# Kernel optimization log

Measured on AMD Instinct MI355X. Metric: run time of the kernel, lower is better.

Reference implementation:

```python
import jax, jax.numpy as jnp
import numpy as np

B, S, C, H = 1, 512, 384, 12
SQK, SV, PQK, PV = 16, 16, 4, 8
SCALAR_SCALE = SQK ** -0.5
NEG = jnp.float32(-10000.0)


def _random_rotations(key, shape):
    # Gram-Schmidt on random normals -> proper rotation matrices (rows orthonormal)
    m = jax.random.normal(key, shape + (3, 3), jnp.float32)
    e0 = m[..., 0, :]
    e0 = e0 / jnp.linalg.norm(e0, axis=-1, keepdims=True)
    e1 = m[..., 1, :] - jnp.sum(e0 * m[..., 1, :], axis=-1, keepdims=True) * e0
    e1 = e1 / jnp.linalg.norm(e1, axis=-1, keepdims=True)
    e2 = jnp.cross(e0, e1)
    return jnp.stack([e0, e1, e2], axis=-2)  # [..., 3, 3]


def setup_inputs() -> dict:
    key = jax.random.key(0)
    ks = jax.random.split(key, 24)
    rn = lambda k, shp, s=1.0: jax.random.normal(k, shp, jnp.float32) * s
    w = 0.02  # weight init scale
    inp = {
        'single_repr': rn(ks[0], (B, S, C)),
        'rotations': _random_rotations(ks[1], (B, S)),
        'translations': rn(ks[2], (B, S, 3), 10.0),
        'Wq_s': rn(ks[3], (C, H * SQK), w), 'bq_s': rn(ks[4], (H * SQK,), w),
        'Wk_s': rn(ks[5], (C, H * SQK), w), 'bk_s': rn(ks[6], (H * SQK,), w),
        'Wv_s': rn(ks[7], (C, H * SV), w), 'bv_s': rn(ks[8], (H * SV,), w),
        'Wq_p': rn(ks[9], (C, H * PQK * 3), w), 'bq_p': rn(ks[10], (H * PQK * 3,), w),
        'Wk_p': rn(ks[11], (C, H * PQK * 3), w), 'bk_p': rn(ks[12], (H * PQK * 3,), w),
        'Wv_p': rn(ks[13], (C, H * PV * 3), w), 'bv_p': rn(ks[14], (H * PV * 3,), w),
        'point_weights': rn(ks[15], (H, PQK), 0.5),
        'Wo': rn(ks[16], (H * (SV + PV * 4), C), w), 'bo': rn(ks[17], (C,), w),
        'valid_mask': jax.random.randint(ks[18], (B, S), 0, 2).astype(bool),
    }
    return inp


def _ipa(single_repr, rotations, translations,
         Wq_s, bq_s, Wk_s, bk_s, Wv_s, bv_s,
         Wq_p, bq_p, Wk_p, bk_p, Wv_p, bv_p,
         point_weights, Wo, bo, valid_mask):
    b, s, _ = single_repr.shape
    qs = (single_repr @ Wq_s + bq_s).reshape(b, s, H, SQK)
    ks = (single_repr @ Wk_s + bk_s).reshape(b, s, H, SQK)
    vs = (single_repr @ Wv_s + bv_s).reshape(b, s, H, SV)
    qp = (single_repr @ Wq_p + bq_p).reshape(b, s, H, PQK, 3)
    kp = (single_repr @ Wk_p + bk_p).reshape(b, s, H, PQK, 3)
    vp = (single_repr @ Wv_p + bv_p).reshape(b, s, H, PV, 3)
    t = translations[:, :, None, None, :]
    # local -> global: R @ p + t
    qpg = jnp.einsum('bsij,bshpj->bshpi', rotations, qp) + t
    kpg = jnp.einsum('bsij,bshpj->bshpi', rotations, kp) + t
    vpg = jnp.einsum('bsij,bshpj->bshpi', rotations, vp) + t
    scalar_logits = jnp.einsum('bihd,bjhd->bhij', qs, ks) * SCALAR_SCALE
    # pairwise point distances: [b, i, j, h, p]
    delta = qpg[:, :, None] - kpg[:, None]  # [b, i, j, h, p, 3]
    dist2 = jnp.sum(delta * delta, axis=-1)
    sp_w = jax.nn.softplus(point_weights)  # [H, PQK]
    point_logits = -0.5 * jnp.einsum('bijhp,hp->bhij', dist2, sp_w)
    logits = scalar_logits + point_logits
    key_mask = valid_mask[:, None, None, :]
    logits = jnp.where(key_mask, logits, NEG)
    attn = jax.nn.softmax(logits, axis=-1)
    attn = attn * valid_mask[:, None, :, None].astype(attn.dtype)
    scalar_out = jnp.einsum('bhij,bjhd->bihd', attn, vs).reshape(b, s, H * SV)
    pog = jnp.einsum('bhij,bjhpd->bihpd', attn, vpg)  # [b, s, H, PV, 3]
    # global -> local: R^T (x - t)
    pol = jnp.einsum('bsji,bshpj->bshpi', rotations, pog - t)
    point_norm = jnp.sqrt(jnp.sum(pol * pol, axis=-1))  # [b, s, H, PV]
    combined = jnp.concatenate([
        scalar_out,
        pol.reshape(b, s, H * PV * 3),
        point_norm.reshape(b, s, H * PV),
    ], axis=-1)
    update = combined @ Wo + bo
    return update * valid_mask[..., None].astype(update.dtype)


def reference(single_repr, rotations, translations,
              Wq_s, bq_s, Wk_s, bk_s, Wv_s, bv_s,
              Wq_p, bq_p, Wk_p, bk_p, Wv_p, bv_p,
              point_weights, Wo, bo, valid_mask):
    return _ipa(single_repr, rotations, translations,
                Wq_s, bq_s, Wk_s, bk_s, Wv_s, bv_s,
                Wq_p, bq_p, Wk_p, bk_p, Wv_p, bv_p,
                point_weights, Wo, bo, valid_mask)
```

## Files before the change

kernel.cpp:

```cpp
#include <hip/hip_runtime.h>
#include <math.h>

#define S 512
#define C 384
#define H 12
#define SCALAR_SCALE 0.25f
#define NEG_LOGIT (-10000.0f)

#define XCOLS 1152
#define DQK 28
#define DV 40

__global__ __launch_bounds__(256)
void gemm_proj(const float* __restrict__ A,
               const float* __restrict__ Wq_s, const float* __restrict__ bq_s,
               const float* __restrict__ Wk_s, const float* __restrict__ bk_s,
               const float* __restrict__ Wv_s, const float* __restrict__ bv_s,
               const float* __restrict__ Wq_p, const float* __restrict__ bq_p,
               const float* __restrict__ Wk_p, const float* __restrict__ bk_p,
               const float* __restrict__ Wv_p, const float* __restrict__ bv_p,
               float* __restrict__ X)
{
    __shared__ float As[48][65];
    __shared__ float Bs[48][65];
    const int tid = threadIdx.x;
    const int m0 = blockIdx.y * 64;
    const int n0 = blockIdx.x * 64;
    const int ty = tid >> 4;
    const int tx = tid & 15;

    const int n = n0 + tx * 4;
    const float* bsrc; const float* bbias; int ldbs, ncol;
    if      (n < 192) { bsrc = Wq_s; bbias = bq_s; ldbs = 192; ncol = n; }
    else if (n < 384) { bsrc = Wk_s; bbias = bk_s; ldbs = 192; ncol = n - 192; }
    else if (n < 576) { bsrc = Wv_s; bbias = bv_s; ldbs = 192; ncol = n - 384; }
    else if (n < 720) { bsrc = Wq_p; bbias = bq_p; ldbs = 144; ncol = n - 576; }
    else if (n < 864) { bsrc = Wk_p; bbias = bk_p; ldbs = 144; ncol = n - 720; }
    else              { bsrc = Wv_p; bbias = bv_p; ldbs = 288; ncol = n - 864; }

    float acc[4][4] = {};

    for (int k0 = 0; k0 < C; k0 += 48) {
        {
            int r = tid >> 2;
            int cbase = (tid & 3) * 4;
            #pragma unroll
            for (int cc = 0; cc < 3; ++cc) {
                int c = cbase + cc * 16;
                const float4 v = *(const float4*)(A + (size_t)(m0 + r) * C + k0 + c);
                As[c + 0][r] = v.x; As[c + 1][r] = v.y;
                As[c + 2][r] = v.z; As[c + 3][r] = v.w;
            }
        }
        {
            int r = tid >> 4;
            int c = tx * 4;
            #pragma unroll
            for (int rr = 0; rr < 3; ++rr) {
                const float4 v = *(const float4*)(bsrc + (size_t)(k0 + r + rr * 16) * ldbs + ncol);
                Bs[r + rr * 16][c + 0] = v.x; Bs[r + rr * 16][c + 1] = v.y;
                Bs[r + rr * 16][c + 2] = v.z; Bs[r + rr * 16][c + 3] = v.w;
            }
        }
        __syncthreads();
        #pragma unroll
        for (int k = 0; k < 48; ++k) {
            float a[4], b[4];
            #pragma unroll
            for (int i = 0; i < 4; ++i) a[i] = As[k][ty * 4 + i];
            #pragma unroll
            for (int j = 0; j < 4; ++j) b[j] = Bs[k][tx * 4 + j];
            #pragma unroll
            for (int i = 0; i < 4; ++i)
                #pragma unroll
                for (int j = 0; j < 4; ++j)
                    acc[i][j] += a[i] * b[j];
        }
        __syncthreads();
    }

    const float4 bb = *(const float4*)(bbias + ncol);
    #pragma unroll
    for (int i = 0; i < 4; ++i) {
        int m = m0 + ty * 4 + i;
        float4 o = make_float4(acc[i][0] + bb.x, acc[i][1] + bb.y,
                               acc[i][2] + bb.z, acc[i][3] + bb.w);
        *(float4*)(X + (size_t)m * XCOLS + n) = o;
    }
}

__global__ __launch_bounds__(256)
void gemm_out(const float* __restrict__ A, int lda,
              const float* __restrict__ B, int ldb,
              const float* __restrict__ bias,
              float* __restrict__ Cc, int ldc, int K,
              const int* __restrict__ rowMask)
{
    __shared__ float As[32][33];
    __shared__ float Bs[32][33];
    const int tid = threadIdx.x;
    const int m0 = blockIdx.y * 32;
    const int n0 = blockIdx.x * 32;
    const int ty = tid >> 4;
    const int tx = tid & 15;

    float acc[2][2] = {};

    for (int k0 = 0; k0 < K; k0 += 32) {
        {
            int r = tid >> 3;
            int c = (tid & 7) * 4;
            const float4 v = *(const float4*)(A + (size_t)(m0 + r) * lda + k0 + c);
            As[c + 0][r] = v.x; As[c + 1][r] = v.y;
            As[c + 2][r] = v.z; As[c + 3][r] = v.w;
        }
        {
            int r = tid >> 3;
            int c = (tid & 7) * 4;
            const float4 v = *(const float4*)(B + (size_t)(k0 + r) * ldb + n0 + c);
            Bs[r][c + 0] = v.x; Bs[r][c + 1] = v.y;
            Bs[r][c + 2] = v.z; Bs[r][c + 3] = v.w;
        }
        __syncthreads();
        #pragma unroll
        for (int k = 0; k < 32; ++k) {
            float a0 = As[k][ty * 2], a1 = As[k][ty * 2 + 1];
            float b0 = Bs[k][tx * 2], b1 = Bs[k][tx * 2 + 1];
            acc[0][0] += a0 * b0; acc[0][1] += a0 * b1;
            acc[1][0] += a1 * b0; acc[1][1] += a1 * b1;
        }
        __syncthreads();
    }

    #pragma unroll
    for (int i = 0; i < 2; ++i) {
        int m = m0 + ty * 2 + i;
        float msk = rowMask[m] ? 1.0f : 0.0f;
        #pragma unroll
        for (int j = 0; j < 2; ++j) {
            int n = n0 + tx * 2 + j;
            Cc[(size_t)m * ldc + n] = (acc[i][j] + bias[n]) * msk;
        }
    }
}

__global__ __launch_bounds__(256)
void ipa_points(const float* __restrict__ X,
                const float* __restrict__ rot,
                const float* __restrict__ trans,
                const float* __restrict__ pw,
                float4* __restrict__ Q4, float4* __restrict__ K4,
                float4* __restrict__ V4, float* __restrict__ kb)
{
    int idx = blockIdx.x * 256 + threadIdx.x;
    int h = idx >> 9;
    int s = idx & 511;

    float R[9], t[3];
    #pragma unroll
    for (int i = 0; i < 9; ++i) R[i] = rot[s * 9 + i];
    #pragma unroll
    for (int i = 0; i < 3; ++i) t[i] = trans[s * 3 + i];

    float spw[4];
    #pragma unroll
    for (int p = 0; p < 4; ++p)
        spw[p] = log1pf(__expf(pw[h * 4 + p]));

    const float4* xr4 = (const float4*)(X + (size_t)s * XCOLS);

    float qv[DQK], kv[DQK], vv[DV];
    #pragma unroll
    for (int g = 0; g < 4; ++g) {
        float4 a = xr4[h * 4 + g];
        qv[g * 4 + 0] = a.x * SCALAR_SCALE; qv[g * 4 + 1] = a.y * SCALAR_SCALE;
        qv[g * 4 + 2] = a.z * SCALAR_SCALE; qv[g * 4 + 3] = a.w * SCALAR_SCALE;
        float4 b = xr4[48 + h * 4 + g];
        kv[g * 4 + 0] = b.x; kv[g * 4 + 1] = b.y; kv[g * 4 + 2] = b.z; kv[g * 4 + 3] = b.w;
        float4 c = xr4[96 + h * 4 + g];
        vv[g * 4 + 0] = c.x; vv[g * 4 + 1] = c.y; vv[g * 4 + 2] = c.z; vv[g * 4 + 3] = c.w;
    }
    float qp[12], kp[12], vp[24];
    #pragma unroll
    for (int g = 0; g < 3; ++g) {
        float4 a = xr4[144 + h * 3 + g];
        qp[g * 4 + 0] = a.x; qp[g * 4 + 1] = a.y; qp[g * 4 + 2] = a.z; qp[g * 4 + 3] = a.w;
        float4 b = xr4[180 + h * 3 + g];
        kp[g * 4 + 0] = b.x; kp[g * 4 + 1] = b.y; kp[g * 4 + 2] = b.z; kp[g * 4 + 3] = b.w;
    }
    #pragma unroll
    for (int g = 0; g < 6; ++g) {
        float4 a = xr4[216 + h * 6 + g];
        vp[g * 4 + 0] = a.x; vp[g * 4 + 1] = a.y; vp[g * 4 + 2] = a.z; vp[g * 4 + 3] = a.w;
    }

    float knorm = 0.0f;
    #pragma unroll
    for (int p = 0; p < 4; ++p) {
        #pragma unroll
        for (int i = 0; i < 3; ++i) {
            float qg = R[i * 3] * qp[p * 3] + R[i * 3 + 1] * qp[p * 3 + 1] + R[i * 3 + 2] * qp[p * 3 + 2] + t[i];
            float kg = R[i * 3] * kp[p * 3] + R[i * 3 + 1] * kp[p * 3 + 1] + R[i * 3 + 2] * kp[p * 3 + 2] + t[i];
            qv[16 + p * 3 + i] = spw[p] * qg;
            kv[16 + p * 3 + i] = kg;
            knorm += spw[p] * kg * kg;
        }
    }
    kb[(size_t)h * S + s] = -0.5f * knorm;

    #pragma unroll
    for (int p = 0; p < 8; ++p) {
        #pragma unroll
        for (int i = 0; i < 3; ++i)
            vv[16 + p * 3 + i] = R[i * 3] * vp[p * 3] + R[i * 3 + 1] * vp[p * 3 + 1] + R[i * 3 + 2] * vp[p * 3 + 2] + t[i];
    }

    #pragma unroll
    for (int g = 0; g < 7; ++g)
        Q4[((size_t)h * 7 + g) * S + s] = make_float4(qv[g * 4], qv[g * 4 + 1], qv[g * 4 + 2], qv[g * 4 + 3]);
    #pragma unroll
    for (int g = 0; g < 7; ++g)
        K4[((size_t)h * 7 + g) * S + s] = make_float4(kv[g * 4], kv[g * 4 + 1], kv[g * 4 + 2], kv[g * 4 + 3]);
    #pragma unroll
    for (int g = 0; g < 10; ++g)
        V4[((size_t)h * 10 + g) * S + s] = make_float4(vv[g * 4], vv[g * 4 + 1], vv[g * 4 + 2], vv[g * 4 + 3]);
}

__global__ __launch_bounds__(256)
void ipa_attn(const float4* __restrict__ Q4, const float4* __restrict__ K4,
              const float4* __restrict__ V4, const float* __restrict__ kb,
              const int* __restrict__ valid,
              const float* __restrict__ rot, const float* __restrict__ trans,
              float* __restrict__ combined)
{
    __shared__ float4 sh[4][10];
    const int h = blockIdx.x;
    const int wave = threadIdx.x >> 6;
    const int lane = threadIdx.x & 63;
    const int i = blockIdx.y * 4 + wave;

    float q[DQK];
    #pragma unroll
    for (int g = 0; g < 7; ++g) {
        float4 v = Q4[((size_t)h * 7 + g) * S + i];
        q[g * 4] = v.x; q[g * 4 + 1] = v.y; q[g * 4 + 2] = v.z; q[g * 4 + 3] = v.w;
    }

    const float* kbh = kb + (size_t)h * S;

    float logit[8];
    float mx = -3.0e38f;
    #pragma unroll
    for (int t = 0; t < 8; ++t) {
        int j = t * 64 + lane;
        float dot = kbh[j];
        #pragma unroll
        for (int g = 0; g < 7; ++g) {
            float4 k = K4[((size_t)h * 7 + g) * S + j];
            dot += q[g * 4] * k.x + q[g * 4 + 1] * k.y + q[g * 4 + 2] * k.z + q[g * 4 + 3] * k.w;
        }
        logit[t] = valid[j] ? dot : NEG_LOGIT;
        mx = fmaxf(mx, logit[t]);
    }
    #pragma unroll
    for (int off = 32; off >= 1; off >>= 1)
        mx = fmaxf(mx, __shfl_xor(mx, off, 64));

    float sum = 0.0f;
    #pragma unroll
    for (int t = 0; t < 8; ++t) {
        logit[t] = __expf(logit[t] - mx);
        sum += logit[t];
    }
    #pragma unroll
    for (int off = 32; off >= 1; off >>= 1)
        sum += __shfl_xor(sum, off, 64);
    const float inv = 1.0f / sum;

    float4 acc[10];
    #pragma unroll
    for (int g = 0; g < 10; ++g) acc[g] = make_float4(0.f, 0.f, 0.f, 0.f);
    #pragma unroll
    for (int t = 0; t < 8; ++t) {
        int j = t * 64 + lane;
        float p = logit[t];
        #pragma unroll
        for (int g = 0; g < 10; ++g) {
            float4 v = V4[((size_t)h * 10 + g) * S + j];
            acc[g].x += p * v.x; acc[g].y += p * v.y;
            acc[g].z += p * v.z; acc[g].w += p * v.w;
        }
    }
    #pragma unroll
    for (int g = 0; g < 10; ++g) {
        #pragma unroll
        for (int off = 32; off >= 1; off >>= 1) {
            acc[g].x += __shfl_xor(acc[g].x, off, 64);
            acc[g].y += __shfl_xor(acc[g].y, off, 64);
            acc[g].z += __shfl_xor(acc[g].z, off, 64);
            acc[g].w += __shfl_xor(acc[g].w, off, 64);
        }
    }

    if (lane == 0) {
        #pragma unroll
        for (int g = 0; g < 10; ++g) sh[wave][g] = acc[g];
    }
    const float* shf = (const float*)sh[wave];

    float* crow = combined + (size_t)i * 576;
    if (lane < 16)
        crow[h * 16 + lane] = shf[lane] * inv;

    if (lane < 8) {
        float R[9], t_[3];
        #pragma unroll
        for (int a = 0; a < 9; ++a) R[a] = rot[i * 9 + a];
        #pragma unroll
        for (int a = 0; a < 3; ++a) t_[a] = trans[i * 3 + a];
        int p = lane;
        float d0 = shf[16 + p * 3 + 0] * inv - t_[0];
        float d1 = shf[16 + p * 3 + 1] * inv - t_[1];
        float d2 = shf[16 + p * 3 + 2] * inv - t_[2];
        float pol0 = R[0] * d0 + R[3] * d1 + R[6] * d2;
        float pol1 = R[1] * d0 + R[4] * d1 + R[7] * d2;
        float pol2 = R[2] * d0 + R[5] * d1 + R[8] * d2;
        crow[192 + h * 24 + p * 3 + 0] = pol0;
        crow[192 + h * 24 + p * 3 + 1] = pol1;
        crow[192 + h * 24 + p * 3 + 2] = pol2;
        crow[480 + h * 8 + p] = sqrtf(pol0 * pol0 + pol1 * pol1 + pol2 * pol2);
    }
}

extern "C" void kernel_launch(void* const* d_in, const int* in_sizes, int n_in,
                              void* d_out, int out_size, void* d_ws, size_t ws_size,
                              hipStream_t stream)
{
    const float* single = (const float*)d_in[0];
    const float* rot    = (const float*)d_in[1];
    const float* trans  = (const float*)d_in[2];
    const float* Wq_s   = (const float*)d_in[3];
    const float* bq_s   = (const float*)d_in[4];
    const float* Wk_s   = (const float*)d_in[5];
    const float* bk_s   = (const float*)d_in[6];
    const float* Wv_s   = (const float*)d_in[7];
    const float* bv_s   = (const float*)d_in[8];
    const float* Wq_p   = (const float*)d_in[9];
    const float* bq_p   = (const float*)d_in[10];
    const float* Wk_p   = (const float*)d_in[11];
    const float* bk_p   = (const float*)d_in[12];
    const float* Wv_p   = (const float*)d_in[13];
    const float* bv_p   = (const float*)d_in[14];
    const float* pw     = (const float*)d_in[15];
    const float* Wo     = (const float*)d_in[16];
    const float* bo     = (const float*)d_in[17];
    const int*   valid  = (const int*)d_in[18];

    float* ws = (float*)d_ws;
    float* X        = ws;
    float* Q4f      = X + (size_t)S * XCOLS;
    float* K4f      = Q4f + (size_t)H * 7 * S * 4;
    float* V4f      = K4f + (size_t)H * 7 * S * 4;
    float* kbb      = V4f + (size_t)H * 10 * S * 4;
    float* combined = kbb + (size_t)H * S;

    dim3 blk(256);

    gemm_proj<<<dim3(XCOLS / 64, S / 64), blk, 0, stream>>>(
        single, Wq_s, bq_s, Wk_s, bk_s, Wv_s, bv_s,
        Wq_p, bq_p, Wk_p, bk_p, Wv_p, bv_p, X);

    ipa_points<<<dim3(S * H / 256), blk, 0, stream>>>(X, rot, trans, pw,
                                                      (float4*)Q4f, (float4*)K4f, (float4*)V4f, kbb);

    ipa_attn<<<dim3(H, S / 4), blk, 0, stream>>>((const float4*)Q4f, (const float4*)K4f,
                                                 (const float4*)V4f, kbb, valid, rot, trans, combined);

    gemm_out<<<dim3(C / 32, S / 32), blk, 0, stream>>>(combined, 576, Wo, C, bo, (float*)d_out, C, 576, valid);
}
```

Before: 189.3 us.

## Split-K projection GEMM with register prefetch; widen output GEMM K tile

Result: no change. 189.1 us (-0.1%).

```diff
diff --git a/kernel.cpp b/kernel.cpp
--- a/kernel.cpp
+++ b/kernel.cpp
@@ -19,13 +19,14 @@
                const float* __restrict__ Wq_p, const float* __restrict__ bq_p,
                const float* __restrict__ Wk_p, const float* __restrict__ bk_p,
                const float* __restrict__ Wv_p, const float* __restrict__ bv_p,
-               float* __restrict__ X)
+               float* __restrict__ X0)
 {
     __shared__ float As[48][65];
     __shared__ float Bs[48][65];
     const int tid = threadIdx.x;
     const int m0 = blockIdx.y * 64;
     const int n0 = blockIdx.x * 64;
+    const int z  = blockIdx.z;
     const int ty = tid >> 4;
     const int tx = tid & 15;
 
@@ -38,31 +39,51 @@
     else if (n < 864) { bsrc = Wk_p; bbias = bk_p; ldbs = 144; ncol = n - 720; }
     else              { bsrc = Wv_p; bbias = bv_p; ldbs = 288; ncol = n - 864; }
 
+    float* Xp = X0 + (size_t)z * S * XCOLS;
+
+    const int ar  = tid >> 2;
+    const int acb = (tid & 3) * 4;
+    const int br  = tid >> 4;
+
+    float4 rA[3], rB[3];
+    {
+        const int k0 = z * 192;
+        #pragma unroll
+        for (int cc = 0; cc < 3; ++cc)
+            rA[cc] = *(const float4*)(A + (size_t)(m0 + ar) * C + k0 + acb + cc * 16);
+        #pragma unroll
+        for (int rr = 0; rr < 3; ++rr)
+            rB[rr] = *(const float4*)(bsrc + (size_t)(k0 + br + rr * 16) * ldbs + ncol);
+    }
+
     float acc[4][4] = {};
 
-    for (int k0 = 0; k0 < C; k0 += 48) {
-        {
-            int r = tid >> 2;
-            int cbase = (tid & 3) * 4;
+    #pragma unroll
+    for (int it = 0; it < 4; ++it) {
+        #pragma unroll
+        for (int cc = 0; cc < 3; ++cc) {
+            int c = acb + cc * 16;
+            As[c + 0][ar] = rA[cc].x; As[c + 1][ar] = rA[cc].y;
+            As[c + 2][ar] = rA[cc].z; As[c + 3][ar] = rA[cc].w;
+        }
+        #pragma unroll
+        for (int rr = 0; rr < 3; ++rr) {
+            int c = tx * 4;
+            Bs[br + rr * 16][c + 0] = rB[rr].x; Bs[br + rr * 16][c + 1] = rB[rr].y;
+            Bs[br + rr * 16][c + 2] = rB[rr].z; Bs[br + rr * 16][c + 3] = rB[rr].w;
+        }
+        __syncthreads();
+
+        if (it < 3) {
+            const int kn = z * 192 + (it + 1) * 48;
             #pragma unroll
-            for (int cc = 0; cc < 3; ++cc) {
-                int c = cbase + cc * 16;
-                const float4 v = *(const float4*)(A + (size_t)(m0 + r) * C + k0 + c);
-                As[c + 0][r] = v.x; As[c + 1][r] = v.y;
-                As[c + 2][r] = v.z; As[c + 3][r] = v.w;
-            }
-        }
-        {
-            int r = tid >> 4;
-            int c = tx * 4;
+            for (int cc = 0; cc < 3; ++cc)
+                rA[cc] = *(const float4*)(A + (size_t)(m0 + ar) * C + kn + acb + cc * 16);
             #pragma unroll
-            for (int rr = 0; rr < 3; ++rr) {
-                const float4 v = *(const float4*)(bsrc + (size_t)(k0 + r + rr * 16) * ldbs + ncol);
-                Bs[r + rr * 16][c + 0] = v.x; Bs[r + rr * 16][c + 1] = v.y;
-                Bs[r + rr * 16][c + 2] = v.z; Bs[r + rr * 16][c + 3] = v.w;
-            }
-        }
-        __syncthreads();
+            for (int rr = 0; rr < 3; ++rr)
+                rB[rr] = *(const float4*)(bsrc + (size_t)(kn + br + rr * 16) * ldbs + ncol);
+        }
+
         #pragma unroll
         for (int k = 0; k < 48; ++k) {
             float a[4], b[4];
@@ -79,13 +100,22 @@
         __syncthreads();
     }
 
-    const float4 bb = *(const float4*)(bbias + ncol);
-    #pragma unroll
-    for (int i = 0; i < 4; ++i) {
-        int m = m0 + ty * 4 + i;
-        float4 o = make_float4(acc[i][0] + bb.x, acc[i][1] + bb.y,
-                               acc[i][2] + bb.z, acc[i][3] + bb.w);
-        *(float4*)(X + (size_t)m * XCOLS + n) = o;
+    if (z == 0) {
+        const float4 bb = *(const float4*)(bbias + ncol);
+        #pragma unroll
+        for (int i = 0; i < 4; ++i) {
+            int m = m0 + ty * 4 + i;
+            *(float4*)(Xp + (size_t)m * XCOLS + n) =
+                make_float4(acc[i][0] + bb.x, acc[i][1] + bb.y,
+                            acc[i][2] + bb.z, acc[i][3] + bb.w);
+        }
+    } else {
+        #pragma unroll
+        for (int i = 0; i < 4; ++i) {
+            int m = m0 + ty * 4 + i;
+            *(float4*)(Xp + (size_t)m * XCOLS + n) =
+                make_float4(acc[i][0], acc[i][1], acc[i][2], acc[i][3]);
+        }
     }
 }
 
@@ -96,8 +126,8 @@
               float* __restrict__ Cc, int ldc, int K,
               const int* __restrict__ rowMask)
 {
-    __shared__ float As[32][33];
-    __shared__ float Bs[32][33];
+    __shared__ float As[48][33];
+    __shared__ float Bs[48][33];
     const int tid = threadIdx.x;
     const int m0 = blockIdx.y * 32;
     const int n0 = blockIdx.x * 32;
@@ -106,24 +136,25 @@
 
     float acc[2][2] = {};
 
-    for (int k0 = 0; k0 < K; k0 += 32) {
-        {
-            int r = tid >> 3;
-            int c = (tid & 7) * 4;
+    for (int k0 = 0; k0 < K; k0 += 48) {
+        for (int idx = tid; idx < 384; idx += 256) {
+            int r  = idx / 12;
+            int c4 = idx - r * 12;
+            int c  = c4 * 4;
             const float4 v = *(const float4*)(A + (size_t)(m0 + r) * lda + k0 + c);
             As[c + 0][r] = v.x; As[c + 1][r] = v.y;
             As[c + 2][r] = v.z; As[c + 3][r] = v.w;
         }
-        {
-            int r = tid >> 3;
-            int c = (tid & 7) * 4;
+        for (int idx = tid; idx < 384; idx += 256) {
+            int r  = idx >> 3;
+            int c  = (idx & 7) * 4;
             const float4 v = *(const float4*)(B + (size_t)(k0 + r) * ldb + n0 + c);
             Bs[r][c + 0] = v.x; Bs[r][c + 1] = v.y;
             Bs[r][c + 2] = v.z; Bs[r][c + 3] = v.w;
         }
         __syncthreads();
         #pragma unroll
-        for (int k = 0; k < 32; ++k) {
+        for (int k = 0; k < 48; ++k) {
             float a0 = As[k][ty * 2], a1 = As[k][ty * 2 + 1];
             float b0 = Bs[k][tx * 2], b1 = Bs[k][tx * 2 + 1];
             acc[0][0] += a0 * b0; acc[0][1] += a0 * b1;
@@ -144,8 +175,14 @@
     }
 }
 
+__device__ __forceinline__ float4 sum2(const float4* a, const float4* b, int i)
+{
+    float4 x = a[i], y = b[i];
+    return make_float4(x.x + y.x, x.y + y.y, x.z + y.z, x.w + y.w);
+}
+
 __global__ __launch_bounds__(256)
-void ipa_points(const float* __restrict__ X,
+void ipa_points(const float* __restrict__ X0,
                 const float* __restrict__ rot,
                 const float* __restrict__ trans,
                 const float* __restrict__ pw,
@@ -167,30 +204,31 @@
     for (int p = 0; p < 4; ++p)
         spw[p] = log1pf(__expf(pw[h * 4 + p]));
 
-    const float4* xr4 = (const float4*)(X + (size_t)s * XCOLS);
+    const float4* xr0 = (const float4*)(X0 + (size_t)s * XCOLS);
+    const float4* xr1 = (const float4*)(X0 + (size_t)S * XCOLS + (size_t)s * XCOLS);
 
     float qv[DQK], kv[DQK], vv[DV];
     #pragma unroll
     for (int g = 0; g < 4; ++g) {
-        float4 a = xr4[h * 4 + g];
+        float4 a = sum2(xr0, xr1, h * 4 + g);
         qv[g * 4 + 0] = a.x * SCALAR_SCALE; qv[g * 4 + 1] = a.y * SCALAR_SCALE;
         qv[g * 4 + 2] = a.z * SCALAR_SCALE; qv[g * 4 + 3] = a.w * SCALAR_SCALE;
-        float4 b = xr4[48 + h * 4 + g];
+        float4 b = sum2(xr0, xr1, 48 + h * 4 + g);
         kv[g * 4 + 0] = b.x; kv[g * 4 + 1] = b.y; kv[g * 4 + 2] = b.z; kv[g * 4 + 3] = b.w;
-        float4 c = xr4[96 + h * 4 + g];
+        float4 c = sum2(xr0, xr1, 96 + h * 4 + g);
         vv[g * 4 + 0] = c.x; vv[g * 4 + 1] = c.y; vv[g * 4 + 2] = c.z; vv[g * 4 + 3] = c.w;
     }
     float qp[12], kp[12], vp[24];
     #pragma unroll
     for (int g = 0; g < 3; ++g) {
-        float4 a = xr4[144 + h * 3 + g];
+        float4 a = sum2(xr0, xr1, 144 + h * 3 + g);
         qp[g * 4 + 0] = a.x; qp[g * 4 + 1] = a.y; qp[g * 4 + 2] = a.z; qp[g * 4 + 3] = a.w;
-        float4 b = xr4[180 + h * 3 + g];
+        float4 b = sum2(xr0, xr1, 180 + h * 3 + g);
         kp[g * 4 + 0] = b.x; kp[g * 4 + 1] = b.y; kp[g * 4 + 2] = b.z; kp[g * 4 + 3] = b.w;
     }
     #pragma unroll
     for (int g = 0; g < 6; ++g) {
-        float4 a = xr4[216 + h * 6 + g];
+        float4 a = sum2(xr0, xr1, 216 + h * 6 + g);
         vp[g * 4 + 0] = a.x; vp[g * 4 + 1] = a.y; vp[g * 4 + 2] = a.z; vp[g * 4 + 3] = a.w;
     }
 
@@ -357,8 +395,8 @@
     const int*   valid  = (const int*)d_in[18];
 
     float* ws = (float*)d_ws;
-    float* X        = ws;
-    float* Q4f      = X + (size_t)S * XCOLS;
+    float* X01      = ws;
+    float* Q4f      = X01 + (size_t)2 * S * XCOLS;
     float* K4f      = Q4f + (size_t)H * 7 * S * 4;
     float* V4f      = K4f + (size_t)H * 7 * S * 4;
     float* kbb      = V4f + (size_t)H * 10 * S * 4;
@@ -366,11 +404,11 @@
 
     dim3 blk(256);
 
-    gemm_proj<<<dim3(XCOLS / 64, S / 64), blk, 0, stream>>>(
+    gemm_proj<<<dim3(XCOLS / 64, S / 64, 2), blk, 0, stream>>>(
         single, Wq_s, bq_s, Wk_s, bk_s, Wv_s, bv_s,
-        Wq_p, bq_p, Wk_p, bk_p, Wv_p, bv_p, X);
-
-    ipa_points<<<dim3(S * H / 256), blk, 0, stream>>>(X, rot, trans, pw,
+        Wq_p, bq_p, Wk_p, bk_p, Wv_p, bv_p, X01);
+
+    ipa_points<<<dim3(S * H / 256), blk, 0, stream>>>(X01, rot, trans, pw,
                                                       (float4*)Q4f, (float4*)K4f, (float4*)V4f, kbb);
 
     ipa_attn<<<dim3(H, S / 4), blk, 0, stream>>>((const float4*)Q4f, (const float4*)K4f,
```
